# Kernel tuning notes

Hardware: AMD Instinct MI355X
Metric: run time of the kernel (lower is better)

Reference implementation:

```python
import jax, jax.numpy as jnp
import numpy as np

L, P, B, C, H, W = 2, 2, 4, 128, 64, 64
K = 2  # negatives per sample


def setup_inputs() -> dict:
    key = jax.random.key(0)
    k1, k2, k3, k4, k5 = jax.random.split(key, 5)
    shp = (L, P, B, C, H, W)
    return {
        "style_E": jax.random.normal(k1, shp, dtype=jnp.float32),
        "style_S": jax.random.normal(k2, shp, dtype=jnp.float32),
        "translate_E": jax.random.normal(k3, shp, dtype=jnp.float32),
        "translate_S": jax.random.normal(k4, shp, dtype=jnp.float32),
        "neg_idx": jax.random.randint(k5, (B, K), 0, B, dtype=jnp.int32),
    }


def reference(style_E, style_S, translate_E, translate_S, neg_idx):
    # Stack E and S levels: [2L, P, B, C, N] with N = H*W
    S = jnp.concatenate([style_E, style_S], axis=0).reshape(2 * L, P, B, C, -1)
    T = jnp.concatenate([translate_E, translate_S], axis=0).reshape(2 * L, P, B, C, -1)

    # EFDM: sort style values; permute them to trans's rank order, then MSE.
    Vs = jnp.sort(S, axis=-1)                      # value_style
    idx_t = jnp.argsort(T, axis=-1)                # index_trans
    inv = jnp.argsort(idx_t, axis=-1)              # inverse_index

    # Positive pairs: style[b] vs trans[b]
    matched_pos = jnp.take_along_axis(Vs, inv, axis=-1)
    # mse over (C, N) per slice (matches mse_loss on a [1,C,N] tensor)
    pos = jnp.mean((T - matched_pos) ** 2, axis=(3, 4))  # [2L, P, B]
    poss_loss = pos.sum(axis=(0, 1))                      # [B]

    # Negatives: style[nb] vs trans[b] for nb in neg_idx[b]
    Vs_neg = Vs[:, :, neg_idx]                            # [2L, P, B, K, C, N]
    matched_neg = jnp.take_along_axis(Vs_neg, inv[:, :, :, None], axis=-1)
    neg = jnp.mean((T[:, :, :, None] - matched_neg) ** 2, axis=(4, 5))  # [2L, P, B, K]
    neg_loss = neg.sum(axis=(0, 1, 3))                    # [B]

    return jnp.sum(poss_loss / neg_loss)
```

## Files before the change

kernel.cpp:

```cpp
#include <hip/hip_runtime.h>


typedef unsigned int u32;
typedef __fp16 f16x2 __attribute__((ext_vector_type(2)));

constexpr int N     = 4096;
constexpr int NTH   = 256;
constexpr int CDIM  = 128;
constexpr int BDIM  = 4;
constexpr int KNEG  = 2;
constexpr int ROWS  = 4096;
constexpr int HALF  = 2048;
constexpr int ROWW  = N / 2;
constexpr int LSTRW = 20;
constexpr int LDSW  = NTH * LSTRW;

__device__ inline int lslot(int t) { return t * LSTRW; }

__device__ inline u32 pk_min(u32 a, u32 b) {
  u32 d; asm("v_pk_min_f16 %0, %1, %2" : "=v"(d) : "v"(a), "v"(b)); return d;
}
__device__ inline u32 pk_max(u32 a, u32 b) {
  u32 d; asm("v_pk_max_f16 %0, %1, %2" : "=v"(d) : "v"(a), "v"(b)); return d;
}
__device__ inline u32 pk_min_negb(u32 a, u32 b) {
  u32 d; asm("v_pk_min_f16 %0, %1, %2 neg_lo:[0,1] neg_hi:[0,1]" : "=v"(d) : "v"(a), "v"(b)); return d;
}
__device__ inline u32 pk_min_swap(u32 a) {
  u32 d; asm("v_pk_min_f16 %0, %1, %1 op_sel:[0,1] op_sel_hi:[1,0]" : "=v"(d) : "v"(a)); return d;
}
__device__ inline u32 pk_max_swap(u32 a) {
  u32 d; asm("v_pk_max_f16 %0, %1, %1 op_sel:[0,1] op_sel_hi:[1,0]" : "=v"(d) : "v"(a)); return d;
}
__device__ inline u32 pk_sub(u32 a, u32 b) {
  u32 d; asm("v_pk_add_f16 %0, %1, %2 neg_lo:[0,1] neg_hi:[0,1]" : "=v"(d) : "v"(a), "v"(b)); return d;
}
__device__ inline float dot2acc(u32 d, float acc) {
  asm("v_dot2_f32_f16 %0, %1, %2, %0" : "+v"(acc) : "v"(d), "v"(d)); return acc;
}

__device__ inline void pk_cswap(u32& a, u32& b) {
  const u32 mn = pk_min(a, b), mx = pk_max(a, b);
  a = mn; b = mx;
}
__device__ inline u32 pk_sort_pair(u32 a) {
  const u32 mn = pk_min_swap(a);
  const u32 mx = pk_max_swap(a);
  return (mx & 0xFFFF0000u) | (mn & 0x0000FFFFu);
}

template<int CTRL>
__device__ inline u32 dpp_u(u32 x) {
  return (u32)__builtin_amdgcn_update_dpp((int)x, (int)x, CTRL, 0xF, 0xF, false);
}
template<int TM>
__device__ inline u32 dppx(u32 x) {
  if constexpr (TM == 1)      return dpp_u<0xB1>(x);
  else if constexpr (TM == 2) return dpp_u<0x4E>(x);
  else if constexpr (TM == 4)
    return (u32)__builtin_amdgcn_ds_swizzle((int)x, 0x101F);
  else                        return dpp_u<0x128>(x);
}

__device__ inline void swap32u(u32& a, u32& b) {
  asm("v_permlane32_swap_b32 %0, %1" : "+v"(a), "+v"(b));
}
__device__ inline void swap16u(u32& a, u32& b) {
  asm("v_permlane16_swap_b32 %0, %1" : "+v"(a), "+v"(b));
}
template<bool IS32>
__device__ inline void pass_perm_pk(u32 h[8]) {
  #pragma unroll
  for (int q = 0; q < 4; ++q) {
    u32 a = h[2*q], b = h[2*q + 1];
    if constexpr (IS32) swap32u(a, b); else swap16u(a, b);
    u32 mn = pk_min(a, b);
    u32 mx = pk_max(a, b);
    if constexpr (IS32) swap32u(mn, mx); else swap16u(mn, mx);
    h[2*q] = mn; h[2*q + 1] = mx;
  }
}

__device__ inline void flip_pk(u32 h[8], u32 f) {
  #pragma unroll
  for (int p = 0; p < 8; ++p) h[p] ^= f;
}

struct PolM { u32 s1, s2, s4, s8; };

template<int TM>
__device__ inline void polar_pass(u32 h[8]) {
  u32 o[8];
  #pragma unroll
  for (int p = 0; p < 8; ++p) o[p] = dppx<TM>(h[p]);
  #pragma unroll
  for (int p = 0; p < 8; ++p) h[p] = pk_min_negb(h[p], o[p]);
}

template<int TMS, bool SKIP_ENTRY>
__device__ inline void polar_block(u32 h[8], const PolM& pm) {
  if constexpr (!SKIP_ENTRY) {
    const u32 e = (TMS == 8) ? pm.s8 : (TMS == 4) ? pm.s4 : (TMS == 2) ? pm.s2 : pm.s1;
    flip_pk(h, e);
  }
  if constexpr (TMS >= 8) { polar_pass<8>(h); flip_pk(h, pm.s8 ^ pm.s4); }
  if constexpr (TMS >= 4) { polar_pass<4>(h); flip_pk(h, pm.s4 ^ pm.s2); }
  if constexpr (TMS >= 2) { polar_pass<2>(h); flip_pk(h, pm.s2 ^ pm.s1); }
  polar_pass<1>(h);
  flip_pk(h, pm.s1);
}

template<int TM>
__device__ inline void pass_lds_pk(u32 h[8], u32* buf, int t) {
  __syncthreads();
  uint4* wp = (uint4*)(buf + lslot(t));
  wp[0] = make_uint4(h[0], h[1], h[2], h[3]);
  wp[1] = make_uint4(h[4], h[5], h[6], h[7]);
  __syncthreads();
  const uint4* rp = (const uint4*)(buf + lslot(t ^ TM));
  const uint4 x0 = rp[0], x1 = rp[1];
  if (t & TM) {
    h[0] = pk_max(h[0], x0.x); h[1] = pk_max(h[1], x0.y);
    h[2] = pk_max(h[2], x0.z); h[3] = pk_max(h[3], x0.w);
    h[4] = pk_max(h[4], x1.x); h[5] = pk_max(h[5], x1.y);
    h[6] = pk_max(h[6], x1.z); h[7] = pk_max(h[7], x1.w);
  } else {
    h[0] = pk_min(h[0], x0.x); h[1] = pk_min(h[1], x0.y);
    h[2] = pk_min(h[2], x0.z); h[3] = pk_min(h[3], x0.w);
    h[4] = pk_min(h[4], x1.x); h[5] = pk_min(h[5], x1.y);
    h[6] = pk_min(h[6], x1.z); h[7] = pk_min(h[7], x1.w);
  }
}

__device__ inline void tail_pk(u32 h[8]) {
  #pragma unroll
  for (int p = 0; p < 8; ++p) h[p] = pk_sort_pair(h[p]);
  pk_cswap(h[0], h[4]); pk_cswap(h[1], h[5]); pk_cswap(h[2], h[6]); pk_cswap(h[3], h[7]);
  pk_cswap(h[0], h[2]); pk_cswap(h[1], h[3]); pk_cswap(h[4], h[6]); pk_cswap(h[5], h[7]);
  pk_cswap(h[0], h[1]); pk_cswap(h[2], h[3]); pk_cswap(h[4], h[5]); pk_cswap(h[6], h[7]);
}

template<int K>
__device__ inline void stage_pk(u32 h[8], u32* buf, int t, u32& cur, const PolM& pm) {
  constexpr bool FOLD = (K >= 32 && K <= 256);
  const u32 f = (K >= 4096) ? 0u : ((t & (K >> 4)) ? 0x80008000u : 0u);
  u32 m = f ^ cur;
  if constexpr (FOLD)
    m ^= (K == 256) ? pm.s8 : (K == 128) ? pm.s4 : (K == 64) ? pm.s2 : pm.s1;
  flip_pk(h, m);
  cur = f;
  if constexpr (K >= 4096) pass_lds_pk<128>(h, buf, t);
  if constexpr (K >= 2048) pass_lds_pk<64>(h, buf, t);
  if constexpr (K >= 1024) pass_perm_pk<true>(h);
  if constexpr (K >= 512)  pass_perm_pk<false>(h);
  if constexpr (K >= 256)      polar_block<8, FOLD>(h, pm);
  else if constexpr (K >= 128) polar_block<4, FOLD>(h, pm);
  else if constexpr (K >= 64)  polar_block<2, FOLD>(h, pm);
  else if constexpr (K >= 32)  polar_block<1, FOLD>(h, pm);
  tail_pk(h);
}

__device__ inline void load_prestage_pack(const float* __restrict__ src,
                                          u32 h[8], int t) {
  float v[16];
  const float4* s4 = (const float4*)src;
  #pragma unroll
  for (int q = 0; q < 4; ++q) {
    const float4 x = s4[t*4 + q];
    v[q*4+0] = x.x; v[q*4+1] = x.y; v[q*4+2] = x.z; v[q*4+3] = x.w;
  }
  #pragma unroll
  for (int p = 0; p < 8; ++p) {
    const f16x2 pk = __builtin_amdgcn_cvt_pkrtz(v[p], v[p + 8]);
    h[p] = __builtin_bit_cast(u32, pk);
  }
  pk_cswap(h[0], h[1]); pk_cswap(h[3], h[2]); pk_cswap(h[4], h[5]); pk_cswap(h[7], h[6]);
  pk_cswap(h[0], h[2]); pk_cswap(h[1], h[3]); pk_cswap(h[6], h[4]); pk_cswap(h[7], h[5]);
  pk_cswap(h[0], h[1]); pk_cswap(h[2], h[3]); pk_cswap(h[5], h[4]); pk_cswap(h[7], h[6]);
  #pragma unroll
  for (int p = 0; p < 8; ++p) h[p] ^= 0x80000000u;
  pk_cswap(h[0], h[4]); pk_cswap(h[1], h[5]); pk_cswap(h[2], h[6]); pk_cswap(h[3], h[7]);
  pk_cswap(h[0], h[2]); pk_cswap(h[1], h[3]); pk_cswap(h[4], h[6]); pk_cswap(h[5], h[7]);
  pk_cswap(h[0], h[1]); pk_cswap(h[2], h[3]); pk_cswap(h[4], h[5]); pk_cswap(h[6], h[7]);
}

__device__ inline void sort4096_pk(u32 h[8], u32* buf, int t, const PolM& pm) {
  u32 cur = 0x80000000u;
  stage_pk<16>(h, buf, t, cur, pm);
  stage_pk<32>(h, buf, t, cur, pm);
  stage_pk<64>(h, buf, t, cur, pm);
  stage_pk<128>(h, buf, t, cur, pm);
  stage_pk<256>(h, buf, t, cur, pm);
  stage_pk<512>(h, buf, t, cur, pm);
  stage_pk<1024>(h, buf, t, cur, pm);
  stage_pk<2048>(h, buf, t, cur, pm);
  stage_pk<4096>(h, buf, t, cur, pm);
}

__global__ __launch_bounds__(NTH)
void sort_one(const float* __restrict__ sE, const float* __restrict__ sS,
              const float* __restrict__ tE, const float* __restrict__ tS,
              u32* __restrict__ Ss, u32* __restrict__ Ts) {
  __shared__ u32 buf[LDSW];
  const int t = threadIdx.x;
  int r = blockIdx.x;
  const float* src;
  u32* dst;
  if (r < ROWS) {
    src = (r < HALF) ? sE + (size_t)r * N : sS + (size_t)(r - HALF) * N;
    dst = Ss + (size_t)r * ROWW;
  } else {
    r -= ROWS;
    src = (r < HALF) ? tE + (size_t)r * N : tS + (size_t)(r - HALF) * N;
    dst = Ts + (size_t)r * ROWW;
  }
  const u32 S = 0x80008000u;
  PolM pm;
  pm.s1 = (t & 1) ? S : 0u;  pm.s2 = (t & 2) ? S : 0u;
  pm.s4 = (t & 4) ? S : 0u;  pm.s8 = (t & 8) ? S : 0u;

  u32 h[8];
  load_prestage_pack(src, h, t);
  sort4096_pk(h, buf, t, pm);
  uint4* d4 = (uint4*)dst;
  d4[t]       = make_uint4(h[0], h[1], h[2], h[3]);
  d4[NTH + t] = make_uint4(h[4], h[5], h[6], h[7]);
}

__global__ __launch_bounds__(NTH)
void diff_rows(const u32* __restrict__ Ss, const u32* __restrict__ Ts,
               const int* __restrict__ neg_idx, float2* __restrict__ partial) {
  __shared__ float red[2][4];
  const int t = threadIdx.x, r = blockIdx.x;

  const uint4* tp = (const uint4*)(Ts + (size_t)r * ROWW);
  const uint4 h0 = tp[t], h1 = tp[NTH + t];

  const int c  = r & (CDIM - 1);
  const int b  = (r / CDIM) & (BDIM - 1);
  const int ap = r / (CDIM * BDIM);

  float posp = 0.f, negp = 0.f;
  {
    const uint4* vp = (const uint4*)(Ss + (size_t)r * ROWW);
    const uint4 w0 = vp[t], w1 = vp[NTH + t];
    posp = dot2acc(pk_sub(h0.x, w0.x), posp);
    posp = dot2acc(pk_sub(h0.y, w0.y), posp);
    posp = dot2acc(pk_sub(h0.z, w0.z), posp);
    posp = dot2acc(pk_sub(h0.w, w0.w), posp);
    posp = dot2acc(pk_sub(h1.x, w1.x), posp);
    posp = dot2acc(pk_sub(h1.y, w1.y), posp);
    posp = dot2acc(pk_sub(h1.z, w1.z), posp);
    posp = dot2acc(pk_sub(h1.w, w1.w), posp);
  }
  #pragma unroll
  for (int k = 0; k < KNEG; ++k) {
    const int nb = neg_idx[b * KNEG + k];
    const uint4* vp = (const uint4*)(Ss + ((size_t)(ap * BDIM + nb) * CDIM + c) * ROWW);
    const uint4 w0 = vp[t], w1 = vp[NTH + t];
    negp = dot2acc(pk_sub(h0.x, w0.x), negp);
    negp = dot2acc(pk_sub(h0.y, w0.y), negp);
    negp = dot2acc(pk_sub(h0.z, w0.z), negp);
    negp = dot2acc(pk_sub(h0.w, w0.w), negp);
    negp = dot2acc(pk_sub(h1.x, w1.x), negp);
    negp = dot2acc(pk_sub(h1.y, w1.y), negp);
    negp = dot2acc(pk_sub(h1.z, w1.z), negp);
    negp = dot2acc(pk_sub(h1.w, w1.w), negp);
  }

  #pragma unroll
  for (int off = 32; off > 0; off >>= 1) {
    posp += __shfl_down(posp, off, 64);
    negp += __shfl_down(negp, off, 64);
  }
  const int wid = t >> 6, lane = t & 63;
  if (lane == 0) { red[0][wid] = posp; red[1][wid] = negp; }
  __syncthreads();
  if (t == 0) {
    const float pt = red[0][0] + red[0][1] + red[0][2] + red[0][3];
    const float nt = red[1][0] + red[1][1] + red[1][2] + red[1][3];
    partial[r] = make_float2(pt, nt);
  }
}

__global__ __launch_bounds__(NTH)
void finalize(const float2* __restrict__ partial, float* __restrict__ out) {
  __shared__ double rp[4], rn[4];
  const int t = threadIdx.x;
  const int wid = t >> 6, lane = t & 63;
  double res = 0.0;
  #pragma unroll
  for (int b = 0; b < BDIM; ++b) {
    double p = 0.0, n = 0.0;
    for (int idx = t; idx < 1024; idx += NTH) {
      const int a = idx >> 7, c = idx & 127;
      const float2 v = partial[a * 512 + b * 128 + c];
      p += (double)v.x; n += (double)v.y;
    }
    #pragma unroll
    for (int off = 32; off > 0; off >>= 1) {
      p += __shfl_down(p, off, 64);
      n += __shfl_down(n, off, 64);
    }
    if (lane == 0) { rp[wid] = p; rn[wid] = n; }
    __syncthreads();
    if (t == 0) {
      const double P = rp[0] + rp[1] + rp[2] + rp[3];
      const double Nn = rn[0] + rn[1] + rn[2] + rn[3];
      res += P / Nn;
    }
    __syncthreads();
  }
  if (t == 0) out[0] = (float)res;
}

extern "C" void kernel_launch(void* const* d_in, const int* in_sizes, int n_in,
                              void* d_out, int out_size, void* d_ws, size_t ws_size,
                              hipStream_t stream) {
  const float* style_E = (const float*)d_in[0];
  const float* style_S = (const float*)d_in[1];
  const float* trans_E = (const float*)d_in[2];
  const float* trans_S = (const float*)d_in[3];
  const int*   neg_idx = (const int*)d_in[4];

  u32*    Ss      = (u32*)d_ws;
  u32*    Ts      = Ss + (size_t)ROWS * ROWW;
  float2* partial = (float2*)(Ts + (size_t)ROWS * ROWW);

  sort_one<<<2 * ROWS, NTH, 0, stream>>>(style_E, style_S, trans_E, trans_S, Ss, Ts);
  diff_rows<<<ROWS, NTH, 0, stream>>>(Ss, Ts, neg_idx, partial);
  finalize<<<1, NTH, 0, stream>>>(partial, (float*)d_out);
}
```

Baseline: 110.6 us.

## Sort style and trans rows together in packed fp16 lanes per block

Each block now sorts one style row and the matching trans row at once, putting the style value in the low fp16 half and the trans value in the high half of each packed register. The old version packed the two halves of a single row and finished each stage with a pair-sort tail. Every thread now holds 16 packed words instead of 8, and the launch uses half as many blocks. This removes the in-word pair sorting and shares the barriers and LDS exchanges between two sorts, in exchange for more registers and a larger LDS write/read per exchange.

```diff
diff --git a/kernel.cpp b/kernel.cpp
--- a/kernel.cpp
+++ b/kernel.cpp
@@ -26,27 +26,15 @@
 __device__ inline u32 pk_min_negb(u32 a, u32 b) {
   u32 d; asm("v_pk_min_f16 %0, %1, %2 neg_lo:[0,1] neg_hi:[0,1]" : "=v"(d) : "v"(a), "v"(b)); return d;
 }
-__device__ inline u32 pk_min_swap(u32 a) {
-  u32 d; asm("v_pk_min_f16 %0, %1, %1 op_sel:[0,1] op_sel_hi:[1,0]" : "=v"(d) : "v"(a)); return d;
-}
-__device__ inline u32 pk_max_swap(u32 a) {
-  u32 d; asm("v_pk_max_f16 %0, %1, %1 op_sel:[0,1] op_sel_hi:[1,0]" : "=v"(d) : "v"(a)); return d;
-}
 __device__ inline u32 pk_sub(u32 a, u32 b) {
   u32 d; asm("v_pk_add_f16 %0, %1, %2 neg_lo:[0,1] neg_hi:[0,1]" : "=v"(d) : "v"(a), "v"(b)); return d;
 }
 __device__ inline float dot2acc(u32 d, float acc) {
   asm("v_dot2_f32_f16 %0, %1, %2, %0" : "+v"(acc) : "v"(d), "v"(d)); return acc;
 }
-
 __device__ inline void pk_cswap(u32& a, u32& b) {
   const u32 mn = pk_min(a, b), mx = pk_max(a, b);
   a = mn; b = mx;
-}
-__device__ inline u32 pk_sort_pair(u32 a) {
-  const u32 mn = pk_min_swap(a);
-  const u32 mx = pk_max_swap(a);
-  return (mx & 0xFFFF0000u) | (mn & 0x0000FFFFu);
 }
 
 template<int CTRL>
@@ -61,17 +49,49 @@
     return (u32)__builtin_amdgcn_ds_swizzle((int)x, 0x101F);
   else                        return dpp_u<0x128>(x);
 }
-
 __device__ inline void swap32u(u32& a, u32& b) {
   asm("v_permlane32_swap_b32 %0, %1" : "+v"(a), "+v"(b));
 }
 __device__ inline void swap16u(u32& a, u32& b) {
   asm("v_permlane16_swap_b32 %0, %1" : "+v"(a), "+v"(b));
 }
+
+__device__ inline void flip16(u32 h[16], u32 f) {
+  #pragma unroll
+  for (int p = 0; p < 16; ++p) h[p] ^= f;
+}
+
+struct PolM { u32 s1, s2, s4, s8; };
+
+template<int TM>
+__device__ inline void polar_pass16(u32 h[16]) {
+  #pragma unroll
+  for (int g = 0; g < 16; g += 8) {
+    u32 o[8];
+    #pragma unroll
+    for (int p = 0; p < 8; ++p) o[p] = dppx<TM>(h[g + p]);
+    #pragma unroll
+    for (int p = 0; p < 8; ++p) h[g + p] = pk_min_negb(h[g + p], o[p]);
+  }
+}
+
+template<int TMS, bool SKIP_ENTRY>
+__device__ inline void polar_block16(u32 h[16], const PolM& pm) {
+  if constexpr (!SKIP_ENTRY) {
+    const u32 e = (TMS == 8) ? pm.s8 : (TMS == 4) ? pm.s4 : (TMS == 2) ? pm.s2 : pm.s1;
+    flip16(h, e);
+  }
+  if constexpr (TMS >= 8) { polar_pass16<8>(h); flip16(h, pm.s8 ^ pm.s4); }
+  if constexpr (TMS >= 4) { polar_pass16<4>(h); flip16(h, pm.s4 ^ pm.s2); }
+  if constexpr (TMS >= 2) { polar_pass16<2>(h); flip16(h, pm.s2 ^ pm.s1); }
+  polar_pass16<1>(h);
+  flip16(h, pm.s1);
+}
+
 template<bool IS32>
-__device__ inline void pass_perm_pk(u32 h[8]) {
-  #pragma unroll
-  for (int q = 0; q < 4; ++q) {
+__device__ inline void pass_perm16(u32 h[16]) {
+  #pragma unroll
+  for (int q = 0; q < 8; ++q) {
     u32 a = h[2*q], b = h[2*q + 1];
     if constexpr (IS32) swap32u(a, b); else swap16u(a, b);
     u32 mn = pk_min(a, b);
@@ -81,150 +101,139 @@
   }
 }
 
-__device__ inline void flip_pk(u32 h[8], u32 f) {
-  #pragma unroll
-  for (int p = 0; p < 8; ++p) h[p] ^= f;
-}
-
-struct PolM { u32 s1, s2, s4, s8; };
-
 template<int TM>
-__device__ inline void polar_pass(u32 h[8]) {
-  u32 o[8];
-  #pragma unroll
-  for (int p = 0; p < 8; ++p) o[p] = dppx<TM>(h[p]);
-  #pragma unroll
-  for (int p = 0; p < 8; ++p) h[p] = pk_min_negb(h[p], o[p]);
-}
-
-template<int TMS, bool SKIP_ENTRY>
-__device__ inline void polar_block(u32 h[8], const PolM& pm) {
-  if constexpr (!SKIP_ENTRY) {
-    const u32 e = (TMS == 8) ? pm.s8 : (TMS == 4) ? pm.s4 : (TMS == 2) ? pm.s2 : pm.s1;
-    flip_pk(h, e);
-  }
-  if constexpr (TMS >= 8) { polar_pass<8>(h); flip_pk(h, pm.s8 ^ pm.s4); }
-  if constexpr (TMS >= 4) { polar_pass<4>(h); flip_pk(h, pm.s4 ^ pm.s2); }
-  if constexpr (TMS >= 2) { polar_pass<2>(h); flip_pk(h, pm.s2 ^ pm.s1); }
-  polar_pass<1>(h);
-  flip_pk(h, pm.s1);
-}
-
-template<int TM>
-__device__ inline void pass_lds_pk(u32 h[8], u32* buf, int t) {
+__device__ inline void pass_lds16(u32 h[16], u32* buf, int t) {
   __syncthreads();
   uint4* wp = (uint4*)(buf + lslot(t));
-  wp[0] = make_uint4(h[0], h[1], h[2], h[3]);
-  wp[1] = make_uint4(h[4], h[5], h[6], h[7]);
+  wp[0] = make_uint4(h[0],  h[1],  h[2],  h[3]);
+  wp[1] = make_uint4(h[4],  h[5],  h[6],  h[7]);
+  wp[2] = make_uint4(h[8],  h[9],  h[10], h[11]);
+  wp[3] = make_uint4(h[12], h[13], h[14], h[15]);
   __syncthreads();
   const uint4* rp = (const uint4*)(buf + lslot(t ^ TM));
-  const uint4 x0 = rp[0], x1 = rp[1];
+  const uint4 x0 = rp[0], x1 = rp[1], x2 = rp[2], x3 = rp[3];
   if (t & TM) {
-    h[0] = pk_max(h[0], x0.x); h[1] = pk_max(h[1], x0.y);
-    h[2] = pk_max(h[2], x0.z); h[3] = pk_max(h[3], x0.w);
-    h[4] = pk_max(h[4], x1.x); h[5] = pk_max(h[5], x1.y);
-    h[6] = pk_max(h[6], x1.z); h[7] = pk_max(h[7], x1.w);
+    h[0]  = pk_max(h[0],  x0.x); h[1]  = pk_max(h[1],  x0.y);
+    h[2]  = pk_max(h[2],  x0.z); h[3]  = pk_max(h[3],  x0.w);
+    h[4]  = pk_max(h[4],  x1.x); h[5]  = pk_max(h[5],  x1.y);
+    h[6]  = pk_max(h[6],  x1.z); h[7]  = pk_max(h[7],  x1.w);
+    h[8]  = pk_max(h[8],  x2.x); h[9]  = pk_max(h[9],  x2.y);
+    h[10] = pk_max(h[10], x2.z); h[11] = pk_max(h[11], x2.w);
+    h[12] = pk_max(h[12], x3.x); h[13] = pk_max(h[13], x3.y);
+    h[14] = pk_max(h[14], x3.z); h[15] = pk_max(h[15], x3.w);
   } else {
-    h[0] = pk_min(h[0], x0.x); h[1] = pk_min(h[1], x0.y);
-    h[2] = pk_min(h[2], x0.z); h[3] = pk_min(h[3], x0.w);
-    h[4] = pk_min(h[4], x1.x); h[5] = pk_min(h[5], x1.y);
-    h[6] = pk_min(h[6], x1.z); h[7] = pk_min(h[7], x1.w);
-  }
-}
-
-__device__ inline void tail_pk(u32 h[8]) {
-  #pragma unroll
-  for (int p = 0; p < 8; ++p) h[p] = pk_sort_pair(h[p]);
-  pk_cswap(h[0], h[4]); pk_cswap(h[1], h[5]); pk_cswap(h[2], h[6]); pk_cswap(h[3], h[7]);
-  pk_cswap(h[0], h[2]); pk_cswap(h[1], h[3]); pk_cswap(h[4], h[6]); pk_cswap(h[5], h[7]);
-  pk_cswap(h[0], h[1]); pk_cswap(h[2], h[3]); pk_cswap(h[4], h[5]); pk_cswap(h[6], h[7]);
+    h[0]  = pk_min(h[0],  x0.x); h[1]  = pk_min(h[1],  x0.y);
+    h[2]  = pk_min(h[2],  x0.z); h[3]  = pk_min(h[3],  x0.w);
+    h[4]  = pk_min(h[4],  x1.x); h[5]  = pk_min(h[5],  x1.y);
+    h[6]  = pk_min(h[6],  x1.z); h[7]  = pk_min(h[7],  x1.w);
+    h[8]  = pk_min(h[8],  x2.x); h[9]  = pk_min(h[9],  x2.y);
+    h[10] = pk_min(h[10], x2.z); h[11] = pk_min(h[11], x2.w);
+    h[12] = pk_min(h[12], x3.x); h[13] = pk_min(h[13], x3.y);
+    h[14] = pk_min(h[14], x3.z); h[15] = pk_min(h[15], x3.w);
+  }
+}
+
+template<int K, int J>
+__device__ inline void local_pass16(u32 h[16]) {
+  #pragma unroll
+  for (int p = 0; p < 16; ++p)
+    if ((p & J) == 0) {
+      if ((p & K) == 0) pk_cswap(h[p], h[p ^ J]);
+      else              pk_cswap(h[p ^ J], h[p]);
+    }
+}
+
+__device__ inline void tail16(u32 h[16]) {
+  #pragma unroll
+  for (int p = 0; p < 16; ++p) if ((p & 8) == 0) pk_cswap(h[p], h[p ^ 8]);
+  #pragma unroll
+  for (int p = 0; p < 16; ++p) if ((p & 4) == 0) pk_cswap(h[p], h[p ^ 4]);
+  #pragma unroll
+  for (int p = 0; p < 16; ++p) if ((p & 2) == 0) pk_cswap(h[p], h[p ^ 2]);
+  #pragma unroll
+  for (int p = 0; p < 16; ++p) if ((p & 1) == 0) pk_cswap(h[p], h[p ^ 1]);
 }
 
 template<int K>
-__device__ inline void stage_pk(u32 h[8], u32* buf, int t, u32& cur, const PolM& pm) {
+__device__ inline void stage16(u32 h[16], u32* buf, int t, u32& cur, const PolM& pm) {
   constexpr bool FOLD = (K >= 32 && K <= 256);
   const u32 f = (K >= 4096) ? 0u : ((t & (K >> 4)) ? 0x80008000u : 0u);
   u32 m = f ^ cur;
   if constexpr (FOLD)
     m ^= (K == 256) ? pm.s8 : (K == 128) ? pm.s4 : (K == 64) ? pm.s2 : pm.s1;
-  flip_pk(h, m);
+  flip16(h, m);
   cur = f;
-  if constexpr (K >= 4096) pass_lds_pk<128>(h, buf, t);
-  if constexpr (K >= 2048) pass_lds_pk<64>(h, buf, t);
-  if constexpr (K >= 1024) pass_perm_pk<true>(h);
-  if constexpr (K >= 512)  pass_perm_pk<false>(h);
-  if constexpr (K >= 256)      polar_block<8, FOLD>(h, pm);
-  else if constexpr (K >= 128) polar_block<4, FOLD>(h, pm);
-  else if constexpr (K >= 64)  polar_block<2, FOLD>(h, pm);
-  else if constexpr (K >= 32)  polar_block<1, FOLD>(h, pm);
-  tail_pk(h);
-}
-
-__device__ inline void load_prestage_pack(const float* __restrict__ src,
-                                          u32 h[8], int t) {
-  float v[16];
-  const float4* s4 = (const float4*)src;
-  #pragma unroll
-  for (int q = 0; q < 4; ++q) {
-    const float4 x = s4[t*4 + q];
-    v[q*4+0] = x.x; v[q*4+1] = x.y; v[q*4+2] = x.z; v[q*4+3] = x.w;
-  }
-  #pragma unroll
-  for (int p = 0; p < 8; ++p) {
-    const f16x2 pk = __builtin_amdgcn_cvt_pkrtz(v[p], v[p + 8]);
-    h[p] = __builtin_bit_cast(u32, pk);
-  }
-  pk_cswap(h[0], h[1]); pk_cswap(h[3], h[2]); pk_cswap(h[4], h[5]); pk_cswap(h[7], h[6]);
-  pk_cswap(h[0], h[2]); pk_cswap(h[1], h[3]); pk_cswap(h[6], h[4]); pk_cswap(h[7], h[5]);
-  pk_cswap(h[0], h[1]); pk_cswap(h[2], h[3]); pk_cswap(h[5], h[4]); pk_cswap(h[7], h[6]);
-  #pragma unroll
-  for (int p = 0; p < 8; ++p) h[p] ^= 0x80000000u;
-  pk_cswap(h[0], h[4]); pk_cswap(h[1], h[5]); pk_cswap(h[2], h[6]); pk_cswap(h[3], h[7]);
-  pk_cswap(h[0], h[2]); pk_cswap(h[1], h[3]); pk_cswap(h[4], h[6]); pk_cswap(h[5], h[7]);
-  pk_cswap(h[0], h[1]); pk_cswap(h[2], h[3]); pk_cswap(h[4], h[5]); pk_cswap(h[6], h[7]);
-}
-
-__device__ inline void sort4096_pk(u32 h[8], u32* buf, int t, const PolM& pm) {
-  u32 cur = 0x80000000u;
-  stage_pk<16>(h, buf, t, cur, pm);
-  stage_pk<32>(h, buf, t, cur, pm);
-  stage_pk<64>(h, buf, t, cur, pm);
-  stage_pk<128>(h, buf, t, cur, pm);
-  stage_pk<256>(h, buf, t, cur, pm);
-  stage_pk<512>(h, buf, t, cur, pm);
-  stage_pk<1024>(h, buf, t, cur, pm);
-  stage_pk<2048>(h, buf, t, cur, pm);
-  stage_pk<4096>(h, buf, t, cur, pm);
+  if constexpr (K >= 4096) pass_lds16<128>(h, buf, t);
+  if constexpr (K >= 2048) pass_lds16<64>(h, buf, t);
+  if constexpr (K >= 1024) pass_perm16<true>(h);
+  if constexpr (K >= 512)  pass_perm16<false>(h);
+  if constexpr (K >= 256)      polar_block16<8, FOLD>(h, pm);
+  else if constexpr (K >= 128) polar_block16<4, FOLD>(h, pm);
+  else if constexpr (K >= 64)  polar_block16<2, FOLD>(h, pm);
+  else if constexpr (K >= 32)  polar_block16<1, FOLD>(h, pm);
+  tail16(h);
 }
 
 __global__ __launch_bounds__(NTH)
-void sort_one(const float* __restrict__ sE, const float* __restrict__ sS,
-              const float* __restrict__ tE, const float* __restrict__ tS,
-              u32* __restrict__ Ss, u32* __restrict__ Ts) {
+void sort_pair(const float* __restrict__ sE, const float* __restrict__ sS,
+               const float* __restrict__ tE, const float* __restrict__ tS,
+               u32* __restrict__ Ss, u32* __restrict__ Ts) {
   __shared__ u32 buf[LDSW];
-  const int t = threadIdx.x;
-  int r = blockIdx.x;
-  const float* src;
-  u32* dst;
-  if (r < ROWS) {
-    src = (r < HALF) ? sE + (size_t)r * N : sS + (size_t)(r - HALF) * N;
-    dst = Ss + (size_t)r * ROWW;
-  } else {
-    r -= ROWS;
-    src = (r < HALF) ? tE + (size_t)r * N : tS + (size_t)(r - HALF) * N;
-    dst = Ts + (size_t)r * ROWW;
-  }
+  const int t = threadIdx.x, r = blockIdx.x;
+  const float* srcS = (r < HALF) ? sE + (size_t)r * N : sS + (size_t)(r - HALF) * N;
+  const float* srcT = (r < HALF) ? tE + (size_t)r * N : tS + (size_t)(r - HALF) * N;
+
+  u32 h[16];
+  {
+    const float4* a4 = (const float4*)srcS;
+    const float4* b4 = (const float4*)srcT;
+    #pragma unroll
+    for (int q = 0; q < 4; ++q) {
+      const float4 xa = a4[t*4 + q];
+      const float4 xb = b4[t*4 + q];
+      const f16x2 p0 = __builtin_amdgcn_cvt_pkrtz(xa.x, xb.x);
+      const f16x2 p1 = __builtin_amdgcn_cvt_pkrtz(xa.y, xb.y);
+      const f16x2 p2 = __builtin_amdgcn_cvt_pkrtz(xa.z, xb.z);
+      const f16x2 p3 = __builtin_amdgcn_cvt_pkrtz(xa.w, xb.w);
+      h[q*4+0] = __builtin_bit_cast(u32, p0);
+      h[q*4+1] = __builtin_bit_cast(u32, p1);
+      h[q*4+2] = __builtin_bit_cast(u32, p2);
+      h[q*4+3] = __builtin_bit_cast(u32, p3);
+    }
+  }
+
+  local_pass16<2, 1>(h);
+  local_pass16<4, 2>(h); local_pass16<4, 1>(h);
+  local_pass16<8, 4>(h); local_pass16<8, 2>(h); local_pass16<8, 1>(h);
+
   const u32 S = 0x80008000u;
   PolM pm;
   pm.s1 = (t & 1) ? S : 0u;  pm.s2 = (t & 2) ? S : 0u;
   pm.s4 = (t & 4) ? S : 0u;  pm.s8 = (t & 8) ? S : 0u;
 
-  u32 h[8];
-  load_prestage_pack(src, h, t);
-  sort4096_pk(h, buf, t, pm);
-  uint4* d4 = (uint4*)dst;
-  d4[t]       = make_uint4(h[0], h[1], h[2], h[3]);
-  d4[NTH + t] = make_uint4(h[4], h[5], h[6], h[7]);
+  u32 cur = 0;
+  stage16<16>(h, buf, t, cur, pm);
+  stage16<32>(h, buf, t, cur, pm);
+  stage16<64>(h, buf, t, cur, pm);
+  stage16<128>(h, buf, t, cur, pm);
+  stage16<256>(h, buf, t, cur, pm);
+  stage16<512>(h, buf, t, cur, pm);
+  stage16<1024>(h, buf, t, cur, pm);
+  stage16<2048>(h, buf, t, cur, pm);
+  stage16<4096>(h, buf, t, cur, pm);
+
+  u32 A[8], B[8];
+  #pragma unroll
+  for (int q = 0; q < 8; ++q) {
+    A[q] = __builtin_amdgcn_perm(h[2*q+1], h[2*q], 0x05040100u);
+    B[q] = __builtin_amdgcn_perm(h[2*q+1], h[2*q], 0x07060302u);
+  }
+  uint4* dA = (uint4*)(Ss + (size_t)r * ROWW);
+  uint4* dB = (uint4*)(Ts + (size_t)r * ROWW);
+  dA[t]       = make_uint4(A[0], A[1], A[2], A[3]);
+  dA[NTH + t] = make_uint4(A[4], A[5], A[6], A[7]);
+  dB[t]       = make_uint4(B[0], B[1], B[2], B[3]);
+  dB[NTH + t] = make_uint4(B[4], B[5], B[6], B[7]);
 }
 
 __global__ __launch_bounds__(NTH)
@@ -327,7 +336,7 @@
   u32*    Ts      = Ss + (size_t)ROWS * ROWW;
   float2* partial = (float2*)(Ts + (size_t)ROWS * ROWW);
 
-  sort_one<<<2 * ROWS, NTH, 0, stream>>>(style_E, style_S, trans_E, trans_S, Ss, Ts);
+  sort_pair<<<ROWS, NTH, 0, stream>>>(style_E, style_S, trans_E, trans_S, Ss, Ts);
   diff_rows<<<ROWS, NTH, 0, stream>>>(Ss, Ts, neg_idx, partial);
   finalize<<<1, NTH, 0, stream>>>(partial, (float*)d_out);
 }
```

New measurement: 104.1 us, median of 2. 5.9% less time.
